# Kernel optimization log

Hardware: AMD Instinct MI355X
Metric: run time of the kernel (lower is better)

Reference implementation:

```python
import jax, jax.numpy as jnp
import numpy as np

B, L_IN, L_CTX, DIM, HEADS = 2, 1536, 256, 1024, 16
HEAD_DIM = DIM // HEADS  # 64
EPS = 1e-6


def _rmsnorm(x, w):
    # RMSNorm over the full inner_dim, matching QKNorm(inner_dim)
    return x * jax.lax.rsqrt(jnp.mean(x * x, axis=-1, keepdims=True) + EPS) * w


def _rope(x, cos, sin):
    # x: (b, n, h, d); cos/sin: (n, d//2); rotate adjacent pairs
    xp = x.reshape(x.shape[:-1] + (HEAD_DIM // 2, 2))
    x1, x2 = xp[..., 0], xp[..., 1]
    c = cos[None, :, None, :]
    s = sin[None, :, None, :]
    out = jnp.stack([x1 * c - x2 * s, x1 * s + x2 * c], axis=-1)
    return out.reshape(x.shape)


def setup_inputs():
    key = jax.random.key(0)
    ks = jax.random.split(key, 12)
    std = 0.02
    inp = jax.random.normal(ks[0], (B, L_IN, DIM), jnp.float32)
    ctx = jax.random.normal(ks[1], (B, L_CTX, DIM), jnp.float32)
    # rope tables over concatenated sequence (context first, then input)
    n = L_CTX + L_IN
    half = HEAD_DIM // 2
    inv_freq = 1.0 / (10000.0 ** (np.arange(half, dtype=np.float32) / half))
    ang = np.arange(n, dtype=np.float32)[:, None] * inv_freq[None, :]
    cos = jnp.asarray(np.cos(ang))
    sin = jnp.asarray(np.sin(ang))
    return {
        "input": inp,
        "context": ctx,
        "cos": cos,
        "sin": sin,
        "Wqkv_in": jax.random.normal(ks[2], (DIM, 3 * DIM), jnp.float32) * std,
        "bqkv_in": jnp.zeros((3 * DIM,), jnp.float32),
        "Wqkv_ctx": jax.random.normal(ks[3], (DIM, 3 * DIM), jnp.float32) * std,
        "bqkv_ctx": jnp.zeros((3 * DIM,), jnp.float32),
        "qw_in": jnp.ones((DIM,), jnp.float32),
        "kw_in": jnp.ones((DIM,), jnp.float32),
        "qw_ctx": jnp.ones((DIM,), jnp.float32),
        "kw_ctx": jnp.ones((DIM,), jnp.float32),
        "Wo_in": jax.random.normal(ks[4], (DIM, DIM), jnp.float32) * std,
        "bo_in": jnp.zeros((DIM,), jnp.float32),
        "Wo_ctx": jax.random.normal(ks[5], (DIM, DIM), jnp.float32) * std,
        "bo_ctx": jnp.zeros((DIM,), jnp.float32),
        "attn_mask": jnp.ones((B, L_CTX), jnp.int32),
    }


def reference(input, context, cos, sin, Wqkv_in, bqkv_in, Wqkv_ctx, bqkv_ctx,
              qw_in, kw_in, qw_ctx, kw_ctx, Wo_in, bo_in, Wo_ctx, bo_ctx, attn_mask):
    # fused QKV projections, then chunk
    qi, ki, vi = jnp.split(input @ Wqkv_in + bqkv_in, 3, axis=-1)
    qc, kc, vc = jnp.split(context @ Wqkv_ctx + bqkv_ctx, 3, axis=-1)
    # QKNorm (RMSNorm over inner_dim)
    qi, ki = _rmsnorm(qi, qw_in), _rmsnorm(ki, kw_in)
    qc, kc = _rmsnorm(qc, qw_ctx), _rmsnorm(kc, kw_ctx)
    # concat context-first, split heads: (b, n, h, d)
    heads = lambda x: x.reshape(B, -1, HEADS, HEAD_DIM)
    q = heads(jnp.concatenate([qc, qi], axis=1))
    k = heads(jnp.concatenate([kc, ki], axis=1))
    v = heads(jnp.concatenate([vc, vi], axis=1))
    # RoPE on q, k (v untouched)
    q = _rope(q, cos, sin)
    k = _rope(k, cos, sin)
    # SDPA: (b, h, n, d)
    q, k, v = (x.transpose(0, 2, 1, 3) for x in (q, k, v))
    scale = HEAD_DIM ** -0.5
    scores = jnp.einsum('bhqd,bhkd->bhqk', q, k) * scale
    full_mask = jnp.concatenate(
        [attn_mask.astype(bool), jnp.ones((B, L_IN), bool)], axis=1)
    scores = jnp.where(full_mask[:, None, None, :], scores,
                       jnp.finfo(scores.dtype).min)
    attn = jax.nn.softmax(scores, axis=-1)
    out = jnp.einsum('bhqk,bhkd->bhqd', attn, v)
    out = out.transpose(0, 2, 1, 3).reshape(B, L_CTX + L_IN, DIM)
    input_output = out[:, L_CTX:, :] @ Wo_in + bo_in
    context_output = out[:, :L_CTX, :] @ Wo_ctx + bo_ctx
    return input_output, context_output
```

## Files before the change

kernel.cpp:

```cpp
#include <hip/hip_runtime.h>
#include <stdint.h>

#define DIMSZ 1024
#define NHEADS 16
#define HD 64
#define BB 2
#define L_IN 1536
#define L_CTX 256
#define NTOT 1792
#define MROWS 3584
#define NT64 (NTOT / 64)

typedef __attribute__((ext_vector_type(8))) short bf16x8;
typedef __attribute__((ext_vector_type(4))) float f32x4;
typedef __attribute__((ext_vector_type(16))) float f32x16;

__device__ inline unsigned short f2bf(float f) {
    union { float f; unsigned u; } v; v.f = f;
    unsigned r = v.u + 0x7fffu + ((v.u >> 16) & 1u);
    return (unsigned short)(r >> 16);
}
__device__ inline float bf2f(unsigned short u) {
    union { float f; unsigned u; } v; v.u = ((unsigned)u) << 16; return v.f;
}
__device__ inline float fexp2(float x) {
    float r;
    asm("v_exp_f32 %0, %1" : "=v"(r) : "v"(x));
    return r;
}

__device__ inline f32x4 zero4() {
    f32x4 v;
    #pragma unroll
    for (int i = 0; i < 4; i++) v[i] = 0.f;
    return v;
}
__device__ inline f32x16 zero16() {
    f32x16 v;
    #pragma unroll
    for (int i = 0; i < 16; i++) v[i] = 0.f;
    return v;
}

#define GLL16(g, l) __builtin_amdgcn_global_load_lds( \
    (const __attribute__((address_space(1))) unsigned int*)(g), \
    (__attribute__((address_space(3))) unsigned int*)(l), 16, 0, 0)

__global__ __launch_bounds__(256) void prep_kernel(
    const float* __restrict__ input, const float* __restrict__ context,
    unsigned short* __restrict__ Abuf,
    const float* __restrict__ Wq_in,  unsigned short* __restrict__ WqT_in,
    const float* __restrict__ Wq_ctx, unsigned short* __restrict__ WqT_ctx,
    const float* __restrict__ Wo_in,  unsigned short* __restrict__ WoT_in,
    const float* __restrict__ Wo_ctx, unsigned short* __restrict__ WoT_ctx)
{
    __shared__ unsigned short sm[64][65];
    int blk = blockIdx.x;
    int t = threadIdx.x;
    if (blk < 3584) {
        int e = (blk * 256 + t) * 4;
        int row = e >> 10, c = e & 1023;
        int b = row / NTOT, ln = row % NTOT;
        const float* src = (ln < L_CTX)
            ? context + ((size_t)b * L_CTX + ln) * 1024 + c
            : input   + ((size_t)b * L_IN + (ln - L_CTX)) * 1024 + c;
        float4 v = *(const float4*)src;
        ushort4 o; o.x = f2bf(v.x); o.y = f2bf(v.y); o.z = f2bf(v.z); o.w = f2bf(v.w);
        *(ushort4*)(Abuf + e) = o;
        return;
    }
    const float* W; unsigned short* Wt; int N; int tb;
    if (blk < 4352)      { W = Wq_in;  Wt = WqT_in;  N = 3072; tb = blk - 3584; }
    else if (blk < 5120) { W = Wq_ctx; Wt = WqT_ctx; N = 3072; tb = blk - 4352; }
    else if (blk < 5376) { W = Wo_in;  Wt = WoT_in;  N = 1024; tb = blk - 5120; }
    else                 { W = Wo_ctx; Wt = WoT_ctx; N = 1024; tb = blk - 5376; }
    int k0 = (tb & 15) * 64, n0 = (tb >> 4) * 64;
    #pragma unroll
    for (int i = 0; i < 4; i++) {
        int r = (t >> 4) + i * 16, c = (t & 15) * 4;
        float4 v = *(const float4*)(W + (size_t)(k0 + r) * N + n0 + c);
        sm[r][c] = f2bf(v.x); sm[r][c + 1] = f2bf(v.y);
        sm[r][c + 2] = f2bf(v.z); sm[r][c + 3] = f2bf(v.w);
    }
    __syncthreads();
    int rn = t & 63, kc = (t >> 6) * 16;
    unsigned short* dst = Wt + (size_t)(n0 + rn) * 1024 + k0 + kc;
    #pragma unroll
    for (int q = 0; q < 4; q++) {
        ushort4 o;
        o.x = sm[kc + q * 4 + 0][rn]; o.y = sm[kc + q * 4 + 1][rn];
        o.z = sm[kc + q * 4 + 2][rn]; o.w = sm[kc + q * 4 + 3][rn];
        *(ushort4*)(dst + q * 4) = o;
    }
}

template<int NLD, bool OUT_BF16, bool IS_QKV>
__global__ __launch_bounds__(256, 4) void gemm3(
    const unsigned short* __restrict__ A,
    const unsigned short* __restrict__ Wt_in, const unsigned short* __restrict__ Wt_ctx,
    const float* __restrict__ bias_in, const float* __restrict__ bias_ctx,
    void* __restrict__ out_in_, void* __restrict__ out_ctx_)
{
    __shared__ __align__(16) char smem[49152];
    const int rt = blockIdx.x, n0 = blockIdx.y * 128;
    const int b = rt / 14, lrt = rt % 14;
    const bool is_ctx = lrt < 2;
    const unsigned short* Wt = is_ctx ? Wt_ctx : Wt_in;
    const float* bias = is_ctx ? bias_ctx : bias_in;
    const int t = threadIdx.x, lane = t & 63, wid = t >> 6;
    const int wr = wid >> 1, wc = wid & 1;
    const int g4 = lane >> 4, l16 = lane & 15;

    const char* asrc[2]; const char* bsrc[2];
    int ldst[2];
    #pragma unroll
    for (int j = 0; j < 2; j++) {
        int o = t * 16 + j * 4096;
        int row = o >> 6;
        int cb = (o & 63) ^ ((row & 3) << 4);
        asrc[j] = (const char*)A  + ((size_t)(rt * 128 + row)) * 2048 + cb;
        bsrc[j] = (const char*)Wt + ((size_t)(n0 + row)) * 2048 + cb;
        ldst[j] = o;
    }

    f32x4 acc[4][4];
    #pragma unroll
    for (int mi = 0; mi < 4; mi++)
        #pragma unroll
        for (int ni = 0; ni < 4; ni++) acc[mi][ni] = zero4();

    auto stage = [&](int kt, int buf) {
        char* base = smem + buf * 16384;
        #pragma unroll
        for (int j = 0; j < 2; j++) {
            GLL16(asrc[j] + kt * 64, base + ldst[j]);
            GLL16(bsrc[j] + kt * 64, base + 8192 + ldst[j]);
        }
    };

    stage(0, 0);
    stage(1, 1);

    int bufc = 0;
    #pragma unroll 1
    for (int kt = 0; kt < 32; kt++) {
        int bufs = bufc + 2; if (bufs >= 3) bufs -= 3;
        stage((kt + 2) & 31, bufs);
        asm volatile("s_waitcnt vmcnt(8)" ::: "memory");
        __builtin_amdgcn_s_barrier();
        const char* base = smem + bufc * 16384;
        bf16x8 a[4], bgf[4];
        #pragma unroll
        for (int mi = 0; mi < 4; mi++) {
            int row = wr * 64 + mi * 16 + l16;
            int byte = row * 64 + ((g4 * 16) ^ ((row & 3) << 4));
            a[mi] = *(const bf16x8*)(base + byte);
        }
        #pragma unroll
        for (int ni = 0; ni < 4; ni++) {
            int row = wc * 64 + ni * 16 + l16;
            int byte = 8192 + row * 64 + ((g4 * 16) ^ ((row & 3) << 4));
            bgf[ni] = *(const bf16x8*)(base + byte);
        }
        #pragma unroll
        for (int mi = 0; mi < 4; mi++)
            #pragma unroll
            for (int ni = 0; ni < 4; ni++)
                acc[mi][ni] = __builtin_amdgcn_mfma_f32_16x16x32_bf16(
                    a[mi], bgf[ni], acc[mi][ni], 0, 0, 0);
        __builtin_amdgcn_s_barrier();
        bufc = bufc + 1; if (bufc >= 3) bufc -= 3;
    }
    asm volatile("s_waitcnt vmcnt(0)" ::: "memory");

    char* optr; size_t orow0;
    if constexpr (IS_QKV) {
        optr = (char*)out_in_; orow0 = (size_t)rt * 128;
    } else {
        if (is_ctx) { optr = (char*)out_ctx_; orow0 = (size_t)b * 256 + lrt * 128; }
        else        { optr = (char*)out_in_;  orow0 = (size_t)b * 1536 + (lrt - 2) * 128; }
    }
    #pragma unroll
    for (int mi = 0; mi < 4; mi++)
        #pragma unroll
        for (int ni = 0; ni < 4; ni++) {
            int col = n0 + wc * 64 + ni * 16 + l16;
            float bv = bias[col];
            #pragma unroll
            for (int r = 0; r < 4; r++) {
                size_t row = orow0 + wr * 64 + mi * 16 + g4 * 4 + r;
                float val = acc[mi][ni][r] + bv;
                if constexpr (OUT_BF16)
                    ((unsigned short*)optr)[row * NLD + col] = f2bf(val);
                else
                    ((float*)optr)[row * NLD + col] = val;
            }
        }
}

__global__ __launch_bounds__(256) void norm_rope_kernel(
    const unsigned short* __restrict__ qkv,
    const float* __restrict__ qw_in, const float* __restrict__ kw_in,
    const float* __restrict__ qw_ctx, const float* __restrict__ kw_ctx,
    const float* __restrict__ cosT, const float* __restrict__ sinT,
    unsigned short* __restrict__ Q, unsigned short* __restrict__ K,
    unsigned short* __restrict__ Vt)
{
    const float QSC = 0.125f * 1.44269504088896f;
    int bn = blockIdx.x;
    int b = bn / NTOT, n = bn % NTOT;
    int t = threadIdx.x;
    const unsigned short* row = qkv + (size_t)bn * 3072;
    ushort4 qu = *(const ushort4*)(row + t * 4);
    ushort4 ku = *(const ushort4*)(row + 1024 + t * 4);
    ushort4 vu = *(const ushort4*)(row + 2048 + t * 4);
    float q0f = bf2f(qu.x), q1f = bf2f(qu.y), q2f = bf2f(qu.z), q3f = bf2f(qu.w);
    float k0f = bf2f(ku.x), k1f = bf2f(ku.y), k2f = bf2f(ku.z), k3f = bf2f(ku.w);
    float sq = q0f * q0f + q1f * q1f + q2f * q2f + q3f * q3f;
    float sk = k0f * k0f + k1f * k1f + k2f * k2f + k3f * k3f;
    #pragma unroll
    for (int m = 1; m < 64; m <<= 1) { sq += __shfl_xor(sq, m); sk += __shfl_xor(sk, m); }
    __shared__ float redq[4], redk[4];
    int lane = t & 63, w = t >> 6;
    if (lane == 0) { redq[w] = sq; redk[w] = sk; }
    __syncthreads();
    sq = redq[0] + redq[1] + redq[2] + redq[3];
    sk = redk[0] + redk[1] + redk[2] + redk[3];
    float rsq = rsqrtf(sq * (1.f / 1024.f) + 1e-6f);
    float rsk = rsqrtf(sk * (1.f / 1024.f) + 1e-6f);
    bool is_ctx = (n < L_CTX);
    const float* qw = is_ctx ? qw_ctx : qw_in;
    const float* kw = is_ctx ? kw_ctx : kw_in;
    int col = t * 4;
    int h = col >> 6, d = col & 63;
    float c0 = cosT[n * 32 + (d >> 1)],     s0 = sinT[n * 32 + (d >> 1)];
    float c1 = cosT[n * 32 + (d >> 1) + 1], s1 = sinT[n * 32 + (d >> 1) + 1];
    size_t base = (((size_t)(b * NHEADS + h)) * NTOT + n) * HD + d;
    {
        float x0 = q0f * rsq * qw[col],     x1 = q1f * rsq * qw[col + 1];
        float x2 = q2f * rsq * qw[col + 2], x3 = q3f * rsq * qw[col + 3];
        float y0 = x0 * c0 - x1 * s0, y1 = x0 * s0 + x1 * c0;
        float y2 = x2 * c1 - x3 * s1, y3 = x2 * s1 + x3 * c1;
        ushort4 o; o.x = f2bf(y0 * QSC); o.y = f2bf(y1 * QSC);
        o.z = f2bf(y2 * QSC); o.w = f2bf(y3 * QSC);
        *(ushort4*)(Q + base) = o;
    }
    {
        float x0 = k0f * rsk * kw[col],     x1 = k1f * rsk * kw[col + 1];
        float x2 = k2f * rsk * kw[col + 2], x3 = k3f * rsk * kw[col + 3];
        float y0 = x0 * c0 - x1 * s0, y1 = x0 * s0 + x1 * c0;
        float y2 = x2 * c1 - x3 * s1, y3 = x2 * s1 + x3 * c1;
        ushort4 o; o.x = f2bf(y0); o.y = f2bf(y1); o.z = f2bf(y2); o.w = f2bf(y3);
        *(ushort4*)(K + base) = o;
    }
    size_t vb = ((size_t)(b * NHEADS + h)) * HD;
    Vt[(vb + d + 0) * NTOT + n] = vu.x;
    Vt[(vb + d + 1) * NTOT + n] = vu.y;
    Vt[(vb + d + 2) * NTOT + n] = vu.z;
    Vt[(vb + d + 3) * NTOT + n] = vu.w;
}

__global__ __launch_bounds__(256) void attn_kernel(
    const unsigned short* __restrict__ Q, const unsigned short* __restrict__ K,
    const unsigned short* __restrict__ Vt, const int* __restrict__ mask,
    unsigned short* __restrict__ Ob)
{
    __shared__ __align__(16) char smem[33792];
    float* mbias = (float*)(smem + 32768);
    int bh = blockIdx.x;
    int b = bh >> 4, h = bh & 15;
    int t = threadIdx.x, lane = t & 63, wid = t >> 6;
    int g = lane >> 5, lq = lane & 31;
    int q0 = blockIdx.y * 128 + wid * 32;

    const unsigned short* Qp = Q + (size_t)bh * NTOT * HD;
    const char* Kbase = (const char*)(K + (size_t)bh * NTOT * HD);
    const char* Vbase = (const char*)(Vt + (size_t)bh * HD * NTOT);

    int srow = wid * 8 + (lane >> 3);
    int srcb = ((lane & 7) * 16) ^ ((lane >> 3) << 4);
    const char* ks0 = Kbase + (size_t)srow * 128 + srcb;
    const char* ks1 = ks0 + 32 * 128;
    const char* vs0 = Vbase + (size_t)srow * (NTOT * 2) + srcb;
    const char* vs1 = vs0 + (size_t)32 * (NTOT * 2);
    const int sdst = wid * 1024 + lane * 16;

    auto stage = [&](int bufbase, int tt) {
        GLL16(ks0 + (size_t)tt * 8192, smem + bufbase + sdst);
        GLL16(ks1 + (size_t)tt * 8192, smem + bufbase + 4096 + sdst);
        GLL16(vs0 + (size_t)tt * 128,  smem + bufbase + 8192 + sdst);
        GLL16(vs1 + (size_t)tt * 128,  smem + bufbase + 8192 + 4096 + sdst);
    };

    stage(0, 0);
    if (t < L_CTX) mbias[t] = mask[b * L_CTX + t] ? 0.f : -1e30f;

    bf16x8 qf[4];
    #pragma unroll
    for (int kk = 0; kk < 4; kk++)
        qf[kk] = *(const bf16x8*)(Qp + (size_t)(q0 + lq) * HD + kk * 16 + g * 8);

    union { unsigned u[4]; bf16x8 v; } onesu;
    #pragma unroll
    for (int i = 0; i < 4; i++) onesu.u[i] = 0x3F803F80u;
    const bf16x8 ones = onesu.v;

    f32x16 oacc0 = zero16(), oacc1 = zero16(), dacc = zero16();
    const int ksw = (lq & 7) << 4;

    auto pack2 = [&](const f32x16& p, bf16x8* pfo) {
        #pragma unroll
        for (int kk = 0; kk < 2; kk++) {
            unsigned a1, b1, a2, b2;
            asm("v_cvt_pk_bf16_f32 %0, %1, %2" : "=v"(a1) : "v"(p[8 * kk + 0]), "v"(p[8 * kk + 1]));
            asm("v_cvt_pk_bf16_f32 %0, %1, %2" : "=v"(a2) : "v"(p[8 * kk + 2]), "v"(p[8 * kk + 3]));
            asm("v_cvt_pk_bf16_f32 %0, %1, %2" : "=v"(b1) : "v"(p[8 * kk + 4]), "v"(p[8 * kk + 5]));
            asm("v_cvt_pk_bf16_f32 %0, %1, %2" : "=v"(b2) : "v"(p[8 * kk + 6]), "v"(p[8 * kk + 7]));
            union { unsigned u[4]; bf16x8 v; } pu;
#if __has_builtin(__builtin_amdgcn_permlane32_swap)
            auto r1 = __builtin_amdgcn_permlane32_swap((int)a1, (int)b1, false, false);
            auto r2 = __builtin_amdgcn_permlane32_swap((int)a2, (int)b2, false, false);
            pu.u[0] = (unsigned)r1[0];
            pu.u[1] = (unsigned)r2[0];
            pu.u[2] = (unsigned)r1[1];
            pu.u[3] = (unsigned)r2[1];
#else
            unsigned sa1 = __shfl_xor(a1, 32), sb1 = __shfl_xor(b1, 32);
            unsigned sa2 = __shfl_xor(a2, 32), sb2 = __shfl_xor(b2, 32);
            pu.u[0] = g ? sb1 : a1;
            pu.u[1] = g ? sb2 : a2;
            pu.u[2] = g ? b1 : sa1;
            pu.u[3] = g ? b2 : sa2;
#endif
            pfo[kk] = pu.v;
        }
    };

    auto compute = [&](const char* bufK, const char* bufV, int kv0, bool msk) {
        f32x16 st0 = zero16(), st1 = zero16();
        #pragma unroll
        for (int kk = 0; kk < 4; kk++) {
            int off = (kk * 32 + g * 16) ^ ksw;
            bf16x8 kf0 = *(const bf16x8*)(bufK + lq * 128 + off);
            bf16x8 kf1 = *(const bf16x8*)(bufK + (lq + 32) * 128 + off);
            st0 = __builtin_amdgcn_mfma_f32_32x32x16_bf16(kf0, qf[kk], st0, 0, 0, 0);
            st1 = __builtin_amdgcn_mfma_f32_32x32x16_bf16(kf1, qf[kk], st1, 0, 0, 0);
        }
        if (msk) {
            #pragma unroll
            for (int r = 0; r < 16; r++) {
                int crow = (r & 3) + 8 * (r >> 2) + 4 * g;
                st0[r] += mbias[kv0 + crow];
                st1[r] += mbias[kv0 + 32 + crow];
            }
        }
        #pragma unroll
        for (int r = 0; r < 16; r++) st0[r] = fexp2(st0[r]);
        #pragma unroll
        for (int r = 0; r < 16; r++) st1[r] = fexp2(st1[r]);
        bf16x8 pf[4];
        pack2(st0, pf);
        pack2(st1, pf + 2);
        #pragma unroll
        for (int kk = 0; kk < 4; kk++) {
            int off = (kk * 32 + g * 16) ^ ksw;
            bf16x8 va = *(const bf16x8*)(bufV + lq * 128 + off);
            bf16x8 vb = *(const bf16x8*)(bufV + (lq + 32) * 128 + off);
            oacc0 = __builtin_amdgcn_mfma_f32_32x32x16_bf16(va, pf[kk], oacc0, 0, 0, 0);
            oacc1 = __builtin_amdgcn_mfma_f32_32x32x16_bf16(vb, pf[kk], oacc1, 0, 0, 0);
            dacc  = __builtin_amdgcn_mfma_f32_32x32x16_bf16(ones, pf[kk], dacc, 0, 0, 0);
        }
    };

    __syncthreads();

    #pragma unroll 1
    for (int tt = 0; tt < NT64; tt++) {
        int curb = (tt & 1) * 16384;
        if (tt + 1 < NT64) stage(16384 - curb, tt + 1);
        compute(smem + curb, smem + curb + 8192, tt * 64, tt < 4);
        __syncthreads();
    }

    float inv = 1.0f / dacc[0];
    int n = q0 + lq;
    size_t obase = ((size_t)(b * NTOT + n)) * DIMSZ + h * HD;
    #pragma unroll
    for (int r = 0; r < 16; r++) {
        int d = (r & 3) + 8 * (r >> 2) + 4 * g;
        Ob[obase + d] = f2bf(oacc0[r] * inv);
        Ob[obase + 32 + d] = f2bf(oacc1[r] * inv);
    }
}

extern "C" void kernel_launch(void* const* d_in, const int* in_sizes, int n_in,
                              void* d_out, int out_size, void* d_ws, size_t ws_size,
                              hipStream_t stream) {
    const float* input    = (const float*)d_in[0];
    const float* context  = (const float*)d_in[1];
    const float* cosT     = (const float*)d_in[2];
    const float* sinT     = (const float*)d_in[3];
    const float* Wqkv_in  = (const float*)d_in[4];
    const float* bqkv_in  = (const float*)d_in[5];
    const float* Wqkv_ctx = (const float*)d_in[6];
    const float* bqkv_ctx = (const float*)d_in[7];
    const float* qw_in    = (const float*)d_in[8];
    const float* kw_in    = (const float*)d_in[9];
    const float* qw_ctx   = (const float*)d_in[10];
    const float* kw_ctx   = (const float*)d_in[11];
    const float* Wo_in    = (const float*)d_in[12];
    const float* bo_in    = (const float*)d_in[13];
    const float* Wo_ctx   = (const float*)d_in[14];
    const float* bo_ctx   = (const float*)d_in[15];
    const int*   mask     = (const int*)d_in[16];

    char* ws = (char*)d_ws;
    unsigned short* WoT_in  = (unsigned short*)(ws);
    unsigned short* WoT_ctx = (unsigned short*)(ws + 2097152);
    unsigned short* qkvb    = (unsigned short*)(ws + 4194304);
    char* U = ws + 26214400;
    unsigned short* Abuf    = (unsigned short*)(U);
    unsigned short* WqT_in  = (unsigned short*)(U + 7340032);
    unsigned short* WqT_ctx = (unsigned short*)(U + 13631488);
    unsigned short* Qb      = (unsigned short*)(U);
    unsigned short* Kb      = (unsigned short*)(U + 7340032);
    unsigned short* Vt      = (unsigned short*)(U + 14680064);
    unsigned short* Ob      = (unsigned short*)(U + 22020096);
    if (ws_size < 64749568) return;

    float* out_in  = (float*)d_out;
    float* out_ctx = out_in + (size_t)BB * L_IN * DIMSZ;

    prep_kernel<<<5632, 256, 0, stream>>>(
        input, context, Abuf,
        Wqkv_in, WqT_in, Wqkv_ctx, WqT_ctx, Wo_in, WoT_in, Wo_ctx, WoT_ctx);

    gemm3<3072, true, true><<<dim3(28, 24), 256, 0, stream>>>(
        Abuf, WqT_in, WqT_ctx, bqkv_in, bqkv_ctx, qkvb, qkvb);

    norm_rope_kernel<<<MROWS, 256, 0, stream>>>(
        qkvb, qw_in, kw_in, qw_ctx, kw_ctx, cosT, sinT, Qb, Kb, Vt);

    attn_kernel<<<dim3(BB * NHEADS, NTOT / 128), 256, 0, stream>>>(
        Qb, Kb, Vt, mask, Ob);

    gemm3<1024, false, false><<<dim3(28, 8), 256, 0, stream>>>(
        Ob, WoT_in, WoT_ctx, bo_in, bo_ctx, out_in, out_ctx);
}
```

Baseline: 137.0 us.

## Process 64 query rows per wave in attention to reuse K/V fragments

The attention kernel now runs 2 waves per block instead of 4, and each wave handles two 32-row query tiles. The K and V fragments read from shared memory feed twice as many MFMAs, which cuts LDS reads per FLOP, and the staging loop is redistributed across 128 threads. The cost is roughly double the accumulator registers per wave, which may lower occupancy, and fewer waves are left to hide load latency and barrier stalls.

```diff
diff --git a/kernel.cpp b/kernel.cpp
--- a/kernel.cpp
+++ b/kernel.cpp
@@ -260,7 +260,7 @@
     Vt[(vb + d + 3) * NTOT + n] = vu.w;
 }
 
-__global__ __launch_bounds__(256) void attn_kernel(
+__global__ __launch_bounds__(128) void attn_kernel(
     const unsigned short* __restrict__ Q, const unsigned short* __restrict__ K,
     const unsigned short* __restrict__ Vt, const int* __restrict__ mask,
     unsigned short* __restrict__ Ob)
@@ -271,41 +271,46 @@
     int b = bh >> 4, h = bh & 15;
     int t = threadIdx.x, lane = t & 63, wid = t >> 6;
     int g = lane >> 5, lq = lane & 31;
-    int q0 = blockIdx.y * 128 + wid * 32;
+    int q0 = blockIdx.y * 128 + wid * 64;
 
     const unsigned short* Qp = Q + (size_t)bh * NTOT * HD;
     const char* Kbase = (const char*)(K + (size_t)bh * NTOT * HD);
     const char* Vbase = (const char*)(Vt + (size_t)bh * HD * NTOT);
-
-    int srow = wid * 8 + (lane >> 3);
-    int srcb = ((lane & 7) * 16) ^ ((lane >> 3) << 4);
-    const char* ks0 = Kbase + (size_t)srow * 128 + srcb;
-    const char* ks1 = ks0 + 32 * 128;
-    const char* vs0 = Vbase + (size_t)srow * (NTOT * 2) + srcb;
-    const char* vs1 = vs0 + (size_t)32 * (NTOT * 2);
-    const int sdst = wid * 1024 + lane * 16;
+    const size_t NT2 = (size_t)NTOT * 2;
+
+    int srow = t >> 3;
+    int srcb = ((t & 7) * 16) ^ ((srow & 7) << 4);
+    const char* ksrc = Kbase + (size_t)srow * 128 + srcb;
+    const char* vsrc = Vbase + (size_t)srow * NT2 + srcb;
+    const int sdst = t * 16;
 
     auto stage = [&](int bufbase, int tt) {
-        GLL16(ks0 + (size_t)tt * 8192, smem + bufbase + sdst);
-        GLL16(ks1 + (size_t)tt * 8192, smem + bufbase + 4096 + sdst);
-        GLL16(vs0 + (size_t)tt * 128,  smem + bufbase + 8192 + sdst);
-        GLL16(vs1 + (size_t)tt * 128,  smem + bufbase + 8192 + 4096 + sdst);
+        #pragma unroll
+        for (int j = 0; j < 4; j++) {
+            GLL16(ksrc + (size_t)tt * 8192 + j * 2048, smem + bufbase + j * 2048 + sdst);
+            GLL16(vsrc + (size_t)tt * 128 + (size_t)j * 16 * NT2,
+                  smem + bufbase + 8192 + j * 2048 + sdst);
+        }
     };
 
     stage(0, 0);
-    if (t < L_CTX) mbias[t] = mask[b * L_CTX + t] ? 0.f : -1e30f;
-
-    bf16x8 qf[4];
-    #pragma unroll
-    for (int kk = 0; kk < 4; kk++)
-        qf[kk] = *(const bf16x8*)(Qp + (size_t)(q0 + lq) * HD + kk * 16 + g * 8);
+    for (int i = t; i < L_CTX; i += 128)
+        mbias[i] = mask[b * L_CTX + i] ? 0.f : -1e30f;
+
+    bf16x8 qfa[4], qfb[4];
+    #pragma unroll
+    for (int kk = 0; kk < 4; kk++) {
+        qfa[kk] = *(const bf16x8*)(Qp + (size_t)(q0 + lq) * HD + kk * 16 + g * 8);
+        qfb[kk] = *(const bf16x8*)(Qp + (size_t)(q0 + 32 + lq) * HD + kk * 16 + g * 8);
+    }
 
     union { unsigned u[4]; bf16x8 v; } onesu;
     #pragma unroll
     for (int i = 0; i < 4; i++) onesu.u[i] = 0x3F803F80u;
     const bf16x8 ones = onesu.v;
 
-    f32x16 oacc0 = zero16(), oacc1 = zero16(), dacc = zero16();
+    f32x16 oacc0a = zero16(), oacc1a = zero16(), dacca = zero16();
+    f32x16 oacc0b = zero16(), oacc1b = zero16(), daccb = zero16();
     const int ksw = (lq & 7) << 4;
 
     auto pack2 = [&](const f32x16& p, bf16x8* pfo) {
@@ -337,38 +342,50 @@
     };
 
     auto compute = [&](const char* bufK, const char* bufV, int kv0, bool msk) {
-        f32x16 st0 = zero16(), st1 = zero16();
+        f32x16 sta0 = zero16(), sta1 = zero16(), stb0 = zero16(), stb1 = zero16();
         #pragma unroll
         for (int kk = 0; kk < 4; kk++) {
             int off = (kk * 32 + g * 16) ^ ksw;
             bf16x8 kf0 = *(const bf16x8*)(bufK + lq * 128 + off);
             bf16x8 kf1 = *(const bf16x8*)(bufK + (lq + 32) * 128 + off);
-            st0 = __builtin_amdgcn_mfma_f32_32x32x16_bf16(kf0, qf[kk], st0, 0, 0, 0);
-            st1 = __builtin_amdgcn_mfma_f32_32x32x16_bf16(kf1, qf[kk], st1, 0, 0, 0);
+            sta0 = __builtin_amdgcn_mfma_f32_32x32x16_bf16(kf0, qfa[kk], sta0, 0, 0, 0);
+            sta1 = __builtin_amdgcn_mfma_f32_32x32x16_bf16(kf1, qfa[kk], sta1, 0, 0, 0);
+            stb0 = __builtin_amdgcn_mfma_f32_32x32x16_bf16(kf0, qfb[kk], stb0, 0, 0, 0);
+            stb1 = __builtin_amdgcn_mfma_f32_32x32x16_bf16(kf1, qfb[kk], stb1, 0, 0, 0);
         }
         if (msk) {
             #pragma unroll
             for (int r = 0; r < 16; r++) {
                 int crow = (r & 3) + 8 * (r >> 2) + 4 * g;
-                st0[r] += mbias[kv0 + crow];
-                st1[r] += mbias[kv0 + 32 + crow];
+                float m0 = mbias[kv0 + crow], m1 = mbias[kv0 + 32 + crow];
+                sta0[r] += m0; sta1[r] += m1;
+                stb0[r] += m0; stb1[r] += m1;
             }
         }
         #pragma unroll
-        for (int r = 0; r < 16; r++) st0[r] = fexp2(st0[r]);
-        #pragma unroll
-        for (int r = 0; r < 16; r++) st1[r] = fexp2(st1[r]);
-        bf16x8 pf[4];
-        pack2(st0, pf);
-        pack2(st1, pf + 2);
+        for (int r = 0; r < 16; r++) sta0[r] = fexp2(sta0[r]);
+        #pragma unroll
+        for (int r = 0; r < 16; r++) sta1[r] = fexp2(sta1[r]);
+        #pragma unroll
+        for (int r = 0; r < 16; r++) stb0[r] = fexp2(stb0[r]);
+        #pragma unroll
+        for (int r = 0; r < 16; r++) stb1[r] = fexp2(stb1[r]);
+        bf16x8 pfa[4], pfb[4];
+        pack2(sta0, pfa);
+        pack2(sta1, pfa + 2);
+        pack2(stb0, pfb);
+        pack2(stb1, pfb + 2);
         #pragma unroll
         for (int kk = 0; kk < 4; kk++) {
             int off = (kk * 32 + g * 16) ^ ksw;
-            bf16x8 va = *(const bf16x8*)(bufV + lq * 128 + off);
-            bf16x8 vb = *(const bf16x8*)(bufV + (lq + 32) * 128 + off);
-            oacc0 = __builtin_amdgcn_mfma_f32_32x32x16_bf16(va, pf[kk], oacc0, 0, 0, 0);
-            oacc1 = __builtin_amdgcn_mfma_f32_32x32x16_bf16(vb, pf[kk], oacc1, 0, 0, 0);
-            dacc  = __builtin_amdgcn_mfma_f32_32x32x16_bf16(ones, pf[kk], dacc, 0, 0, 0);
+            bf16x8 va  = *(const bf16x8*)(bufV + lq * 128 + off);
+            bf16x8 vbv = *(const bf16x8*)(bufV + (lq + 32) * 128 + off);
+            oacc0a = __builtin_amdgcn_mfma_f32_32x32x16_bf16(va,  pfa[kk], oacc0a, 0, 0, 0);
+            oacc1a = __builtin_amdgcn_mfma_f32_32x32x16_bf16(vbv, pfa[kk], oacc1a, 0, 0, 0);
+            oacc0b = __builtin_amdgcn_mfma_f32_32x32x16_bf16(va,  pfb[kk], oacc0b, 0, 0, 0);
+            oacc1b = __builtin_amdgcn_mfma_f32_32x32x16_bf16(vbv, pfb[kk], oacc1b, 0, 0, 0);
+            dacca  = __builtin_amdgcn_mfma_f32_32x32x16_bf16(ones, pfa[kk], dacca, 0, 0, 0);
+            daccb  = __builtin_amdgcn_mfma_f32_32x32x16_bf16(ones, pfb[kk], daccb, 0, 0, 0);
         }
     };
 
@@ -382,14 +399,18 @@
         __syncthreads();
     }
 
-    float inv = 1.0f / dacc[0];
-    int n = q0 + lq;
-    size_t obase = ((size_t)(b * NTOT + n)) * DIMSZ + h * HD;
+    float inva = 1.0f / dacca[0];
+    float invb = 1.0f / daccb[0];
+    int na = q0 + lq, nb = q0 + 32 + lq;
+    size_t obA = ((size_t)(b * NTOT + na)) * DIMSZ + h * HD;
+    size_t obB = ((size_t)(b * NTOT + nb)) * DIMSZ + h * HD;
     #pragma unroll
     for (int r = 0; r < 16; r++) {
         int d = (r & 3) + 8 * (r >> 2) + 4 * g;
-        Ob[obase + d] = f2bf(oacc0[r] * inv);
-        Ob[obase + 32 + d] = f2bf(oacc1[r] * inv);
+        Ob[obA + d]      = f2bf(oacc0a[r] * inva);
+        Ob[obA + 32 + d] = f2bf(oacc1a[r] * inva);
+        Ob[obB + d]      = f2bf(oacc0b[r] * invb);
+        Ob[obB + 32 + d] = f2bf(oacc1b[r] * invb);
     }
 }
 
@@ -441,7 +462,7 @@
     norm_rope_kernel<<<MROWS, 256, 0, stream>>>(
         qkvb, qw_in, kw_in, qw_ctx, kw_ctx, cosT, sinT, Qb, Kb, Vt);
 
-    attn_kernel<<<dim3(BB * NHEADS, NTOT / 128), 256, 0, stream>>>(
+    attn_kernel<<<dim3(BB * NHEADS, NTOT / 128), 128, 0, stream>>>(
         Qb, Kb, Vt, mask, Ob);
 
     gemm3<1024, false, false><<<dim3(28, 8), 256, 0, stream>>>(
```

Result: no change. 139.2 us (+1.6%).
